# Optimization experiments

Measured on AMD Instinct MI355X. Metric: run time of the kernel, lower is better.

## Reference

```python
import jax, jax.numpy as jnp
import numpy as np

B, L, N, D, H, R = 4, 4096, 1024, 768, 12, 8
HD = D // H
LORA_SCALE = 16.0 / 8.0
EPS = 1e-5

def _layernorm(x, g, b):
    mu = jnp.mean(x, axis=-1, keepdims=True)
    var = jnp.mean(jnp.square(x - mu), axis=-1, keepdims=True)
    return (x - mu) * jax.lax.rsqrt(var + EPS) * g + b

def setup_inputs() -> dict:
    key = jax.random.key(0)
    ks = jax.random.split(key, 16)
    s = 0.02
    return {
        "text": jax.random.normal(ks[0], (B, L, D), jnp.float32),
        "regions": jax.random.normal(ks[1], (B, N, D), jnp.float32),
        "region_mask": jax.random.randint(ks[2], (B, N), 0, 2) > 0,
        "Wq": jax.random.normal(ks[3], (D, D), jnp.float32) * s,
        "Aq": jax.random.normal(ks[4], (R, D), jnp.float32) * s,
        "Bq": jax.random.normal(ks[5], (D, R), jnp.float32) * s,
        "Wk": jax.random.normal(ks[6], (D, D), jnp.float32) * s,
        "Wv": jax.random.normal(ks[7], (D, D), jnp.float32) * s,
        "Av": jax.random.normal(ks[8], (R, D), jnp.float32) * s,
        "Bv": jax.random.normal(ks[9], (D, R), jnp.float32) * s,
        "Wo": jax.random.normal(ks[10], (D, D), jnp.float32) * s,
        "bo": jnp.zeros((D,), jnp.float32),
        "gq": jnp.ones((D,), jnp.float32),
        "bq_ln": jnp.zeros((D,), jnp.float32),
        "gkv": jnp.ones((D,), jnp.float32),
        "bkv": jnp.zeros((D,), jnp.float32),
    }

def reference(text, regions, region_mask, Wq, Aq, Bq, Wk, Wv, Av, Bv, Wo, bo, gq, bq_ln, gkv, bkv):
    # pre-norms
    tq = _layernorm(text, gq, bq_ln)          # (B,L,D)
    rk = _layernorm(regions, gkv, bkv)        # (B,N,D)
    # LoRA-adapted projections (weights stored as (out,in), torch convention)
    Q = tq @ Wq.T + LORA_SCALE * ((tq @ Aq.T) @ Bq.T)
    K = rk @ Wk.T
    V = regions @ Wv.T + LORA_SCALE * ((regions @ Av.T) @ Bv.T)
    Q = Q.reshape(B, L, H, HD)
    K = K.reshape(B, N, H, HD)
    V = V.reshape(B, N, H, HD)
    scale = HD ** -0.5
    attn = jnp.einsum('blhd,bnhd->bhln', Q, K) * scale   # (B,H,L,N)
    bad = ~region_mask[:, None, None, :]
    attn = jnp.where(bad, -jnp.inf, attn)
    attn = jax.nn.softmax(attn, axis=-1)
    attn = jnp.nan_to_num(attn, nan=0.0)                 # fully-masked rows -> 0
    # dropout: eval mode (identity)
    out = jnp.einsum('bhln,bnhd->blhd', attn, V).reshape(B, L, D)
    return text + out @ Wo.T + bo
```

## Files before the change

kernel.cpp:

```cpp
#include <hip/hip_runtime.h>
#include <cstdint>
#include <cstddef>

#define B_  4
#define L_  4096
#define N_  1024
#define D_  768
#define H_  12
#define HD_ 64

typedef __bf16 bf16x4 __attribute__((ext_vector_type(4)));
typedef __bf16 bf16x8 __attribute__((ext_vector_type(8)));
typedef float  f32x4  __attribute__((ext_vector_type(4)));
typedef unsigned int u32;

static __device__ __forceinline__ f32x4 mfma16(bf16x8 a, bf16x8 b, f32x4 c) {
    return __builtin_amdgcn_mfma_f32_16x16x32_bf16(a, b, c, 0, 0, 0);
}

static __device__ __forceinline__ void async_cp16(const __bf16* g, const __bf16* l) {
    __builtin_amdgcn_global_load_lds(
        (const __attribute__((address_space(1))) u32*)g,
        (__attribute__((address_space(3))) u32*)l, 16, 0, 0);
}

static __device__ __forceinline__ u32 pkbf(float lo, float hi) {
    union { __bf16 b[2]; u32 u; } r;
    r.b[0] = (__bf16)lo; r.b[1] = (__bf16)hi;
    return r.u;
}


static __device__ __forceinline__ void ln_row(const float* __restrict__ xr,
                                              const float* __restrict__ g,
                                              const float* __restrict__ be,
                                              __bf16* __restrict__ yr)
{
    const int tid = threadIdx.x, lane = tid & 63, wid = tid >> 6;
    float4 v = make_float4(0.f, 0.f, 0.f, 0.f);
    if (tid < 192) v = *(const float4*)(xr + tid * 4);
    float s  = v.x + v.y + v.z + v.w;
    float s2 = v.x * v.x + v.y * v.y + v.z * v.z + v.w * v.w;
#pragma unroll
    for (int off = 32; off > 0; off >>= 1) {
        s  += __shfl_down(s, off);
        s2 += __shfl_down(s2, off);
    }
    __shared__ float red[8];
    if (lane == 0) { red[wid] = s; red[4 + wid] = s2; }
    __syncthreads();
    s  = red[0] + red[1] + red[2] + red[3];
    s2 = red[4] + red[5] + red[6] + red[7];
    const float mean = s * (1.f / D_);
    const float var  = s2 * (1.f / D_) - mean * mean;
    const float rstd = rsqrtf(var + 1e-5f);
    if (tid < 192) {
        const float4 gv = *(const float4*)(g + tid * 4);
        const float4 bv = *(const float4*)(be + tid * 4);
        bf16x4 o;
        o[0] = (__bf16)((v.x - mean) * rstd * gv.x + bv.x);
        o[1] = (__bf16)((v.y - mean) * rstd * gv.y + bv.y);
        o[2] = (__bf16)((v.z - mean) * rstd * gv.z + bv.z);
        o[3] = (__bf16)((v.w - mean) * rstd * gv.w + bv.w);
        *(bf16x4*)(yr + tid * 4) = o;
    }
}

static __device__ __forceinline__ void ln_cast_region(const float* __restrict__ xr,
                                                      const int* __restrict__ maskb, int n,
                                                      const float* __restrict__ g,
                                                      const float* __restrict__ be,
                                                      __bf16* __restrict__ rk_base,
                                                      __bf16* __restrict__ regb_base)
{
    const int tid = threadIdx.x, lane = tid & 63, wid = tid >> 6;
    const bool keep = maskb[n] != 0;

    __shared__ int cnt[4];
    int pos = 0;
    for (int i0 = 0; i0 < n; i0 += 256) {
        const int i = i0 + tid;
        const int mv = (i < n) ? maskb[i] : 0;
        const unsigned long long bal = __ballot(mv != 0);
        if (lane == 0) cnt[wid] = __popcll(bal);
        __syncthreads();
        pos += cnt[0] + cnt[1] + cnt[2] + cnt[3];
        __syncthreads();
    }
    if (!keep) return;

    float4 v = make_float4(0.f, 0.f, 0.f, 0.f);
    if (tid < 192) v = *(const float4*)(xr + tid * 4);
    float s  = v.x + v.y + v.z + v.w;
    float s2 = v.x * v.x + v.y * v.y + v.z * v.z + v.w * v.w;
#pragma unroll
    for (int off = 32; off > 0; off >>= 1) {
        s  += __shfl_down(s, off);
        s2 += __shfl_down(s2, off);
    }
    __shared__ float red[8];
    if (lane == 0) { red[wid] = s; red[4 + wid] = s2; }
    __syncthreads();
    s  = red[0] + red[1] + red[2] + red[3];
    s2 = red[4] + red[5] + red[6] + red[7];
    const float mean = s * (1.f / D_);
    const float var  = s2 * (1.f / D_) - mean * mean;
    const float rstd = rsqrtf(var + 1e-5f);
    if (tid < 192) {
        const float4 gv = *(const float4*)(g + tid * 4);
        const float4 bv = *(const float4*)(be + tid * 4);
        bf16x4 o, c;
        o[0] = (__bf16)((v.x - mean) * rstd * gv.x + bv.x);
        o[1] = (__bf16)((v.y - mean) * rstd * gv.y + bv.y);
        o[2] = (__bf16)((v.z - mean) * rstd * gv.z + bv.z);
        o[3] = (__bf16)((v.w - mean) * rstd * gv.w + bv.w);
        c[0] = (__bf16)v.x; c[1] = (__bf16)v.y; c[2] = (__bf16)v.z; c[3] = (__bf16)v.w;
        *(bf16x4*)(rk_base + (size_t)pos * D_ + tid * 4) = o;
        *(bf16x4*)(regb_base + (size_t)pos * D_ + tid * 4) = c;
    }
}

static __device__ __forceinline__ void cast4(const float* __restrict__ in,
                                             __bf16* __restrict__ out, int blk)
{
    const int i = (blk * 256 + threadIdx.x) * 4;
    const float4 v = *(const float4*)(in + i);
    bf16x4 o;
    o[0] = (__bf16)v.x; o[1] = (__bf16)v.y; o[2] = (__bf16)v.z; o[3] = (__bf16)v.w;
    *(bf16x4*)(out + i) = o;
}

static __device__ __forceinline__ void weff4(const float* __restrict__ W,
                                             const float* __restrict__ Bm,
                                             const float* __restrict__ Am,
                                             __bf16* __restrict__ out, int blk)
{
    const int idx = (blk * 256 + threadIdx.x) * 4;
    const int o = idx / D_, i = idx - o * D_;
    const float4 w = *(const float4*)(W + idx);
    float sx = 0.f, sy = 0.f, sz = 0.f, sw = 0.f;
#pragma unroll
    for (int r = 0; r < 8; ++r) {
        const float b = Bm[o * 8 + r];
        const float4 a = *(const float4*)(Am + r * D_ + i);
        sx += b * a.x; sy += b * a.y; sz += b * a.z; sw += b * a.w;
    }
    bf16x4 ov;
    ov[0] = (__bf16)(w.x + 2.f * sx);
    ov[1] = (__bf16)(w.y + 2.f * sy);
    ov[2] = (__bf16)(w.z + 2.f * sz);
    ov[3] = (__bf16)(w.w + 2.f * sw);
    *(bf16x4*)(out + idx) = ov;
}

static __device__ __forceinline__ void count_mask(const int* __restrict__ maskb,
                                                  int* __restrict__ Nv)
{
    const int tid = threadIdx.x, lane = tid & 63, wid = tid >> 6;
    const int4 mv = *(const int4*)(maskb + tid * 4);
    int c = (mv.x != 0) + (mv.y != 0) + (mv.z != 0) + (mv.w != 0);
#pragma unroll
    for (int off = 32; off > 0; off >>= 1) c += __shfl_down(c, off);
    __shared__ int w4[4];
    if (lane == 0) w4[wid] = c;
    __syncthreads();
    if (tid == 0) *Nv = w4[0] + w4[1] + w4[2] + w4[3];
}

__global__ __launch_bounds__(256) void prologue_kernel(
    const float* __restrict__ text, const float* __restrict__ regions,
    const int* __restrict__ mask,
    const float* __restrict__ Wq, const float* __restrict__ Aq, const float* __restrict__ Bq,
    const float* __restrict__ Wv, const float* __restrict__ Av, const float* __restrict__ Bv,
    const float* __restrict__ Wk, const float* __restrict__ Wo,
    const float* __restrict__ gq, const float* __restrict__ bq,
    const float* __restrict__ gkv, const float* __restrict__ bkv,
    __bf16* __restrict__ tq, __bf16* __restrict__ rk, __bf16* __restrict__ regb,
    __bf16* __restrict__ Weq, __bf16* __restrict__ Wev,
    __bf16* __restrict__ Wkb, __bf16* __restrict__ Wob,
    int* __restrict__ NvArr)
{
    int bx = blockIdx.x;
    if (bx < B_ * L_) { ln_row(text + (size_t)bx * D_, gq, bq, tq + (size_t)bx * D_); return; }
    bx -= B_ * L_;
    if (bx < B_ * N_) {
        const int b = bx >> 10, n = bx & (N_ - 1);
        ln_cast_region(regions + (size_t)bx * D_, mask + b * N_, n, gkv, bkv,
                       rk + (size_t)b * N_ * D_, regb + (size_t)b * N_ * D_);
        return;
    }
    bx -= B_ * N_;
    if (bx < 576) { weff4(Wq, Bq, Aq, Weq, bx); return; }
    bx -= 576;
    if (bx < 576) { weff4(Wv, Bv, Av, Wev, bx); return; }
    bx -= 576;
    if (bx < 576) { cast4(Wk, Wkb, bx); return; }
    bx -= 576;
    if (bx < 576) { cast4(Wo, Wob, bx); return; }
    bx -= 576;
    count_mask(mask + bx * N_, NvArr + bx);
}

template <int EPI, typename CT>
static __device__ __forceinline__ void gemm_body(__bf16* sm,
                                                 const __bf16* __restrict__ A,
                                                 const __bf16* __restrict__ W,
                                                 CT* __restrict__ C,
                                                 const float* __restrict__ resid,
                                                 const float* __restrict__ bias,
                                                 int mb0, int nb0)
{
    const int tid = threadIdx.x, wid = tid >> 6, lane = tid & 63;
    const int lr = lane & 15, g = lane >> 4;
    const int wm = wid >> 1, wn = wid & 1;

    auto skey2 = [](int row) { return (row >> 1) & 3; };

    auto stage = [&](int kb, int buf) {
        __bf16* as = sm + buf * 8192;
        __bf16* bs = as + 4096;
#pragma unroll
        for (int j = 0; j < 2; ++j) {
            const int s = wid * 64 + lane + j * 256;
            const int row = s >> 2;
            const int c = (s & 3) ^ skey2(row);
            const int dst = (wid * 64 + j * 256) * 8;
            async_cp16(A + (size_t)(mb0 + row) * D_ + kb * 32 + c * 8, as + dst);
            async_cp16(W + (size_t)(nb0 + row) * D_ + kb * 32 + c * 8, bs + dst);
        }
    };

    f32x4 acc[4][4] = {};

    stage(0, 0);
    asm volatile("s_waitcnt vmcnt(0)" ::: "memory");
    __syncthreads();

    for (int kb = 0; kb < D_ / 32; ++kb) {
        const int buf = kb & 1;
        if (kb < D_ / 32 - 1) stage(kb + 1, buf ^ 1);
        const __bf16* as = sm + buf * 8192;
        const __bf16* bs = as + 4096;
        bf16x8 av[4], wv[4];
#pragma unroll
        for (int mi = 0; mi < 4; ++mi) {
            const int row = wm * 64 + mi * 16 + lr;
            av[mi] = *(const bf16x8*)(as + row * 32 + (g ^ skey2(row)) * 8);
        }
#pragma unroll
        for (int oi = 0; oi < 4; ++oi) {
            const int row = wn * 64 + oi * 16 + lr;
            wv[oi] = *(const bf16x8*)(bs + row * 32 + (g ^ skey2(row)) * 8);
        }
        __builtin_amdgcn_s_setprio(1);
#pragma unroll
        for (int mi = 0; mi < 4; ++mi)
#pragma unroll
            for (int oi = 0; oi < 4; ++oi)
                acc[mi][oi] = mfma16(av[mi], wv[oi], acc[mi][oi]);
        __builtin_amdgcn_s_setprio(0);
        asm volatile("s_waitcnt vmcnt(0)" ::: "memory");
        __syncthreads();
    }

#pragma unroll
    for (int mi = 0; mi < 4; ++mi) {
#pragma unroll
        for (int oi = 0; oi < 4; ++oi) {
#pragma unroll
            for (int r = 0; r < 4; ++r) {
                const int m = mb0 + wm * 64 + mi * 16 + g * 4 + r;
                const int o = nb0 + wn * 64 + oi * 16 + lr;
                float v = acc[mi][oi][r];
                if (EPI == 2)
                    v += resid[(size_t)m * D_ + o] + bias[o];
                if (EPI == 3)
                    v *= 0.125f;
                if (EPI == 1) {
                    const size_t idx =
                        ((size_t)((m >> 10) * H_ + (o >> 6)) * HD_ + (o & 63)) * N_ + (m & (N_ - 1));
                    C[idx] = (CT)v;
                } else {
                    C[(size_t)m * D_ + o] = (CT)v;
                }
            }
        }
    }
}

__global__ __launch_bounds__(256) void gemm_qkv(const __bf16* __restrict__ tq,
                                                const __bf16* __restrict__ Weq,
                                                __bf16* __restrict__ Qb,
                                                const __bf16* __restrict__ rk,
                                                const __bf16* __restrict__ Wkb,
                                                __bf16* __restrict__ Kb,
                                                const __bf16* __restrict__ regb,
                                                const __bf16* __restrict__ Wev,
                                                __bf16* __restrict__ Vt,
                                                const int* __restrict__ NvArr)
{
    extern __shared__ __bf16 smem[];
    const int gid = blockIdx.x;
    if (gid < 768) {
        const int xcd = gid & 7, pos = gid >> 3;
        const int s = xcd * 96 + pos;
        gemm_body<3, __bf16>(smem, tq, Weq, Qb, nullptr, nullptr, (s / 6) * 128, (s % 6) * 128);
    } else if (gid < 960) {
        const int lin = gid - 768;
        const int m0 = (lin / 6) * 128, ny = (lin % 6) * 128;
        if ((m0 & (N_ - 1)) >= NvArr[m0 >> 10]) return;
        gemm_body<0, __bf16>(smem, rk, Wkb, Kb, nullptr, nullptr, m0, ny);
    } else {
        const int lin = gid - 960;
        const int m0 = (lin / 6) * 128, ny = (lin % 6) * 128;
        if ((m0 & (N_ - 1)) >= NvArr[m0 >> 10]) return;
        gemm_body<1, __bf16>(smem, regb, Wev, Vt, nullptr, nullptr, m0, ny);
    }
}

__global__ __launch_bounds__(256) void gemm_out(const __bf16* __restrict__ A,
                                                const __bf16* __restrict__ W,
                                                float* __restrict__ C,
                                                const float* __restrict__ resid,
                                                const float* __restrict__ bias)
{
    extern __shared__ __bf16 smem[];
    const int xcd = blockIdx.x & 7, pos = blockIdx.x >> 3;
    const int s = xcd * 96 + pos;
    gemm_body<2, float>(smem, A, W, C, resid, bias, (s / 6) * 128, (s % 6) * 128);
}

__global__ __launch_bounds__(256, 3) void attn_kernel(const __bf16* __restrict__ Qb,
                                                      const __bf16* __restrict__ Kb,
                                                      const __bf16* __restrict__ Vt,
                                                      const int* __restrict__ NvArr,
                                                      __bf16* __restrict__ ctx)
{
    const int bq = blockIdx.x, h = blockIdx.y, b = blockIdx.z;
    const int tid = threadIdx.x, wid = tid >> 6, lane = tid & 63;
    const int lr = lane & 15, g = lane >> 4;

    const int Nv = NvArr[b];
    const int ntiles = (Nv + 63) >> 6;

    __shared__ float maskadd[N_];
    __shared__ __align__(16) __bf16 kbuf[2][4096];
    __shared__ __align__(16) __bf16 vbuf[2][4096];

    for (int i = tid; i < N_; i += 256)
        maskadd[i] = (i < Nv) ? 0.f : -1e30f;

    const int hoff = h * HD_;
    const int bN = b * N_;
    const size_t bhHD = ((size_t)b * H_ + h) * HD_;

    auto skey = [](int row) { return (row & 3) | (((row >> 3) & 1) << 2); };

    auto stage = [&](int t, int bsel) {
        const int n0 = t * 64;
#pragma unroll
        for (int j = 0; j < 2; ++j) {
            const int s = wid * 64 + lane + j * 256;
            const int row = s >> 3;
            const int ks = (s & 7) ^ skey(row);
            const int dst = (wid * 64 + j * 256) * 8;
            async_cp16(Kb + ((size_t)(bN + n0 + row) * D_ + hoff + ks * 8), &kbuf[bsel][dst]);
            async_cp16(Vt + (bhHD + row) * N_ + n0 + ks * 8, &vbuf[bsel][dst]);
        }
    };

    const int q0 = bq * 128 + wid * 32;
    bf16x8 qa[2][2];
#pragma unroll
    for (int qf = 0; qf < 2; ++qf) {
        const __bf16* qptr = Qb + ((size_t)b * L_ + q0 + qf * 16 + lr) * D_ + hoff + g * 8;
        qa[qf][0] = *(const bf16x8*)(qptr);
        qa[qf][1] = *(const bf16x8*)(qptr + 32);
    }

    f32x4 acc[2][4] = {};
    float ssum[2] = {0.f, 0.f};

    if (ntiles > 0) {
        stage(0, 0);
        asm volatile("s_waitcnt vmcnt(0)" ::: "memory");
        __syncthreads();

        for (int t = 0; t < ntiles; ++t) {
            const int buf = t & 1;
            if (t + 1 < ntiles) stage(t + 1, buf ^ 1);

            const __bf16* kb = kbuf[buf];
            const __bf16* vb = vbuf[buf];

            f32x4 mv[4];
#pragma unroll
            for (int kt = 0; kt < 4; ++kt)
                mv[kt] = *(const f32x4*)&maskadd[t * 64 + (kt >> 1) * 32 + g * 8 + (kt & 1) * 4];

            bf16x8 kf[4][2];
#pragma unroll
            for (int kt = 0; kt < 4; ++kt) {
                const int row = (kt >> 1) * 32 + (lr >> 2) * 8 + (kt & 1) * 4 + (lr & 3);
                const int kx = skey(row);
#pragma unroll
                for (int kc = 0; kc < 2; ++kc)
                    kf[kt][kc] = *(const bf16x8*)((const char*)kb + row * 128 + ((((kc * 4) + g) ^ kx) << 4));
            }

            bf16x8 pa[2][2];
#pragma unroll
            for (int qf = 0; qf < 2; ++qf) {
                f32x4 s4[4];
                __builtin_amdgcn_s_setprio(1);
#pragma unroll
                for (int kt = 0; kt < 4; ++kt) {
                    f32x4 z = {};
                    s4[kt] = mfma16(kf[kt][0], qa[qf][0], z);
                    s4[kt] = mfma16(kf[kt][1], qa[qf][1], s4[kt]);
                }
                __builtin_amdgcn_s_setprio(0);

                float p[4][4];
                float tsum = 0.f;
#pragma unroll
                for (int kt = 0; kt < 4; ++kt)
#pragma unroll
                    for (int r = 0; r < 4; ++r) {
                        p[kt][r] = __expf(s4[kt][r] + mv[kt][r]);
                        tsum += p[kt][r];
                    }
                tsum += __shfl_xor(tsum, 16);
                tsum += __shfl_xor(tsum, 32);
                ssum[qf] += tsum;

#pragma unroll
                for (int c = 0; c < 2; ++c) {
                    union { u32 w[4]; bf16x8 v; } pu;
#pragma unroll
                    for (int m = 0; m < 4; ++m) {
                        const int kt = 2 * c + (m >> 1);
                        pu.w[m] = pkbf(p[kt][2 * (m & 1)], p[kt][2 * (m & 1) + 1]);
                    }
                    pa[qf][c] = pu.v;
                }
            }

            __builtin_amdgcn_s_setprio(1);
#pragma unroll
            for (int dt = 0; dt < 4; ++dt) {
                const int d = dt * 16 + lr;
                const int vx = skey(d);
#pragma unroll
                for (int c = 0; c < 2; ++c) {
                    const bf16x8 vf = *(const bf16x8*)((const char*)vb + d * 128 + ((((c * 4) + g) ^ vx) << 4));
                    acc[0][dt] = mfma16(pa[0][c], vf, acc[0][dt]);
                    acc[1][dt] = mfma16(pa[1][c], vf, acc[1][dt]);
                }
            }
            __builtin_amdgcn_s_setprio(0);

            asm volatile("s_waitcnt vmcnt(0)" ::: "memory");
            __syncthreads();
        }
    }

#pragma unroll
    for (int qf = 0; qf < 2; ++qf) {
        const float inv = (ssum[qf] > 0.f) ? 1.f / ssum[qf] : 0.f;
        float iv[4];
#pragma unroll
        for (int r = 0; r < 4; ++r) iv[r] = __shfl(inv, g * 4 + r);
#pragma unroll
        for (int dt = 0; dt < 4; ++dt)
#pragma unroll
            for (int r = 0; r < 4; ++r) {
                const int q = q0 + qf * 16 + g * 4 + r;
                ctx[((size_t)b * L_ + q) * D_ + hoff + dt * 16 + lr] = (__bf16)(acc[qf][dt][r] * iv[r]);
            }
    }
}

extern "C" void kernel_launch(void* const* d_in, const int* in_sizes, int n_in,
                              void* d_out, int out_size, void* d_ws, size_t ws_size,
                              hipStream_t stream)
{
    const float* text    = (const float*)d_in[0];
    const float* regions = (const float*)d_in[1];
    const int*   mask    = (const int*)d_in[2];
    const float* Wq  = (const float*)d_in[3];
    const float* Aq  = (const float*)d_in[4];
    const float* Bq  = (const float*)d_in[5];
    const float* Wk  = (const float*)d_in[6];
    const float* Wv  = (const float*)d_in[7];
    const float* Av  = (const float*)d_in[8];
    const float* Bv  = (const float*)d_in[9];
    const float* Wo  = (const float*)d_in[10];
    const float* bo  = (const float*)d_in[11];
    const float* gq  = (const float*)d_in[12];
    const float* bq  = (const float*)d_in[13];
    const float* gkv = (const float*)d_in[14];
    const float* bkv = (const float*)d_in[15];

    const size_t BLD = (size_t)B_ * L_ * D_;
    const size_t BND = (size_t)B_ * N_ * D_;
    const size_t DD  = (size_t)D_ * D_;
    __bf16* ws   = (__bf16*)d_ws;
    __bf16* tq   = ws;
    __bf16* rk   = tq + BLD;
    __bf16* Qb   = rk + BND;
    __bf16* Kb   = Qb + BLD;
    __bf16* Vt   = Kb + BND;
    __bf16* ctx  = Vt + BND;
    __bf16* regb = ctx + BLD;
    __bf16* Weq  = regb + BND;
    __bf16* Wev  = Weq + DD;
    __bf16* Wkb  = Wev + DD;
    __bf16* Wob  = Wkb + DD;
    int* NvArr   = (int*)(Wob + DD);

    const int smB = 32768;
    const int nProBlocks = B_ * L_ + B_ * N_ + 576 * 4 + B_;

    prologue_kernel<<<dim3(nProBlocks), 256, 0, stream>>>(
        text, regions, mask, Wq, Aq, Bq, Wv, Av, Bv, Wk, Wo,
        gq, bq, gkv, bkv, tq, rk, regb, Weq, Wev, Wkb, Wob, NvArr);
    gemm_qkv<<<dim3(1152), 256, smB, stream>>>(tq, Weq, Qb, rk, Wkb, Kb, regb, Wev, Vt, NvArr);
    attn_kernel<<<dim3(L_ / 128, H_, B_), 256, 0, stream>>>(Qb, Kb, Vt, NvArr, ctx);
    gemm_out<<<dim3(768), 256, smB, stream>>>(ctx, Wob, (float*)d_out, text, bo);
}
```

Baseline: 145.7 us.

## Triple-buffer GEMM staging and drop shared mask array in attention

The GEMM main loop moves from double to triple buffering. Two stages are issued ahead, a partial vmcnt wait is used, and there is one barrier per step instead of two. In attention, the shared-memory additive mask is removed: the mask is applied only on the last tile with an index compare, and occupancy is raised to 4 blocks per CU. The aim is to overlap global loads with MFMA work and cut per-tile LDS reads, at the cost of more GEMM shared memory (48KB) and tighter register limits in attention.

Measured after the change: 180.0 us. +23.5%, slower.

```diff
diff --git a/kernel.cpp b/kernel.cpp
--- a/kernel.cpp
+++ b/kernel.cpp
@@ -213,6 +213,7 @@
     const int tid = threadIdx.x, wid = tid >> 6, lane = tid & 63;
     const int lr = lane & 15, g = lane >> 4;
     const int wm = wid >> 1, wn = wid & 1;
+    const int NSTEP = D_ / 32;
 
     auto skey2 = [](int row) { return (row >> 1) & 3; };
 
@@ -233,13 +234,16 @@
     f32x4 acc[4][4] = {};
 
     stage(0, 0);
-    asm volatile("s_waitcnt vmcnt(0)" ::: "memory");
-    __syncthreads();
-
-    for (int kb = 0; kb < D_ / 32; ++kb) {
-        const int buf = kb & 1;
-        if (kb < D_ / 32 - 1) stage(kb + 1, buf ^ 1);
-        const __bf16* as = sm + buf * 8192;
+    stage(1, 1);
+
+    for (int kb = 0; kb < NSTEP; ++kb) {
+        if (kb < NSTEP - 1) asm volatile("s_waitcnt vmcnt(4)" ::: "memory");
+        else                asm volatile("s_waitcnt vmcnt(0)" ::: "memory");
+        __builtin_amdgcn_s_barrier();
+
+        if (kb + 2 < NSTEP) stage(kb + 2, (kb + 2) % 3);
+
+        const __bf16* as = sm + (kb % 3) * 8192;
         const __bf16* bs = as + 4096;
         bf16x8 av[4], wv[4];
 #pragma unroll
@@ -259,8 +263,6 @@
             for (int oi = 0; oi < 4; ++oi)
                 acc[mi][oi] = mfma16(av[mi], wv[oi], acc[mi][oi]);
         __builtin_amdgcn_s_setprio(0);
-        asm volatile("s_waitcnt vmcnt(0)" ::: "memory");
-        __syncthreads();
     }
 
 #pragma unroll
@@ -330,7 +332,7 @@
     gemm_body<2, float>(smem, A, W, C, resid, bias, (s / 6) * 128, (s % 6) * 128);
 }
 
-__global__ __launch_bounds__(256, 3) void attn_kernel(const __bf16* __restrict__ Qb,
+__global__ __launch_bounds__(256, 4) void attn_kernel(const __bf16* __restrict__ Qb,
                                                       const __bf16* __restrict__ Kb,
                                                       const __bf16* __restrict__ Vt,
                                                       const int* __restrict__ NvArr,
@@ -343,12 +345,8 @@
     const int Nv = NvArr[b];
     const int ntiles = (Nv + 63) >> 6;
 
-    __shared__ float maskadd[N_];
     __shared__ __align__(16) __bf16 kbuf[2][4096];
     __shared__ __align__(16) __bf16 vbuf[2][4096];
-
-    for (int i = tid; i < N_; i += 256)
-        maskadd[i] = (i < Nv) ? 0.f : -1e30f;
 
     const int hoff = h * HD_;
     const int bN = b * N_;
@@ -393,11 +391,6 @@
             const __bf16* kb = kbuf[buf];
             const __bf16* vb = vbuf[buf];
 
-            f32x4 mv[4];
-#pragma unroll
-            for (int kt = 0; kt < 4; ++kt)
-                mv[kt] = *(const f32x4*)&maskadd[t * 64 + (kt >> 1) * 32 + g * 8 + (kt & 1) * 4];
-
             bf16x8 kf[4][2];
 #pragma unroll
             for (int kt = 0; kt < 4; ++kt) {
@@ -407,6 +400,8 @@
                 for (int kc = 0; kc < 2; ++kc)
                     kf[kt][kc] = *(const bf16x8*)((const char*)kb + row * 128 + ((((kc * 4) + g) ^ kx) << 4));
             }
+
+            const bool lastTile = (t == ntiles - 1);
 
             bf16x8 pa[2][2];
 #pragma unroll
@@ -423,13 +418,26 @@
 
                 float p[4][4];
                 float tsum = 0.f;
-#pragma unroll
-                for (int kt = 0; kt < 4; ++kt)
-#pragma unroll
-                    for (int r = 0; r < 4; ++r) {
-                        p[kt][r] = __expf(s4[kt][r] + mv[kt][r]);
-                        tsum += p[kt][r];
+                if (lastTile) {
+#pragma unroll
+                    for (int kt = 0; kt < 4; ++kt) {
+                        const int jb = t * 64 + (kt >> 1) * 32 + g * 8 + (kt & 1) * 4;
+#pragma unroll
+                        for (int r = 0; r < 4; ++r) {
+                            const float e = __expf(s4[kt][r]);
+                            p[kt][r] = (jb + r < Nv) ? e : 0.f;
+                            tsum += p[kt][r];
+                        }
                     }
+                } else {
+#pragma unroll
+                    for (int kt = 0; kt < 4; ++kt)
+#pragma unroll
+                        for (int r = 0; r < 4; ++r) {
+                            p[kt][r] = __expf(s4[kt][r]);
+                            tsum += p[kt][r];
+                        }
+                }
                 tsum += __shfl_xor(tsum, 16);
                 tsum += __shfl_xor(tsum, 32);
                 ssum[qf] += tsum;
@@ -519,7 +527,7 @@
     __bf16* Wob  = Wkb + DD;
     int* NvArr   = (int*)(Wob + DD);
 
-    const int smB = 32768;
+    const int smB = 49152;
     const int nProBlocks = B_ * L_ + B_ * N_ + 576 * 4 + B_;
 
     prologue_kernel<<<dim3(nProBlocks), 256, 0, stream>>>(
```
